# Kernel tuning notes

Hardware: AMD Instinct MI355X
Metric: run time of the kernel (lower is better)

Reference implementation:

```python
import jax, jax.numpy as jnp
import numpy as np

B = 1 << 20
EMB = 8
N_BREEDS, N_TEMPS = 15, 9
HIDDENS = [128, 64, 32]
IN_DIM = (EMB * 2 + 9) * 2  # 50
EPS = 1e-5


def _encode_pet(breed, size, energy, temp, age, social, weight, breed_emb, temp_emb):
    # breed/temp: [B] int -> embedding gather [B,8]; size/energy -> one-hot [B,3]
    be = breed_emb[breed]
    te = temp_emb[temp]
    size_oh = jax.nn.one_hot(size, 3, dtype=be.dtype)
    energy_oh = jax.nn.one_hot(energy, 3, dtype=be.dtype)
    nums = jnp.stack([age / 15.0, social, weight / 100.0], axis=-1)  # [B,3]
    return jnp.concatenate([be, size_oh, energy_oh, te, nums], axis=-1)  # [B,25]


def _mlp(x, Ws, bs, gammas, betas, Wout, bout):
    for W, b, g, bt in zip(Ws, bs, gammas, betas):
        x = x @ W + b
        mu = jnp.mean(x, axis=0)
        var = jnp.mean(jnp.square(x - mu), axis=0)  # biased var (torch BN training)
        x = (x - mu) * jax.lax.rsqrt(var + EPS) * g + bt
        x = jax.nn.relu(x)
    x = x @ Wout + bout
    return jax.nn.sigmoid(x).squeeze(-1)  # [B]


def setup_inputs() -> dict:
    key = jax.random.key(0)
    ks = jax.random.split(key, 32)
    inp = {
        "pet1_breed": jax.random.randint(ks[0], (B,), 0, N_BREEDS, dtype=jnp.int32),
        "pet1_size": jax.random.randint(ks[1], (B,), 0, 3, dtype=jnp.int32),
        "pet1_energy": jax.random.randint(ks[2], (B,), 0, 3, dtype=jnp.int32),
        "pet1_temp": jax.random.randint(ks[3], (B,), 0, N_TEMPS, dtype=jnp.int32),
        "pet1_age": jax.random.uniform(ks[4], (B,)) * 15.0,
        "pet1_social": jax.random.uniform(ks[5], (B,)),
        "pet1_weight": jax.random.uniform(ks[6], (B,)) * 100.0,
        "pet2_breed": jax.random.randint(ks[7], (B,), 0, N_BREEDS, dtype=jnp.int32),
        "pet2_size": jax.random.randint(ks[8], (B,), 0, 3, dtype=jnp.int32),
        "pet2_energy": jax.random.randint(ks[9], (B,), 0, 3, dtype=jnp.int32),
        "pet2_temp": jax.random.randint(ks[10], (B,), 0, N_TEMPS, dtype=jnp.int32),
        "pet2_age": jax.random.uniform(ks[11], (B,)) * 15.0,
        "pet2_social": jax.random.uniform(ks[12], (B,)),
        "pet2_weight": jax.random.uniform(ks[13], (B,)) * 100.0,
        "breed_emb": jax.random.normal(ks[14], (N_BREEDS, EMB), dtype=jnp.float32),
        "temp_emb": jax.random.normal(ks[15], (N_TEMPS, EMB), dtype=jnp.float32),
    }
    prev = IN_DIM
    ki = 16
    for i, h in enumerate(HIDDENS, start=1):
        s = 1.0 / np.sqrt(prev)
        inp[f"W{i}"] = jax.random.uniform(ks[ki], (prev, h), minval=-s, maxval=s); ki += 1
        inp[f"b{i}"] = jax.random.uniform(ks[ki], (h,), minval=-s, maxval=s); ki += 1
        inp[f"gamma{i}"] = jnp.ones((h,), jnp.float32)
        inp[f"beta{i}"] = jnp.zeros((h,), jnp.float32)
        prev = h
    s = 1.0 / np.sqrt(prev)
    inp["W4"] = jax.random.uniform(ks[ki], (prev, 1), minval=-s, maxval=s); ki += 1
    inp["b4"] = jax.random.uniform(ks[ki], (1,), minval=-s, maxval=s)
    return inp


def reference(pet1_breed, pet1_size, pet1_energy, pet1_temp, pet1_age, pet1_social, pet1_weight,
              pet2_breed, pet2_size, pet2_energy, pet2_temp, pet2_age, pet2_social, pet2_weight,
              breed_emb, temp_emb,
              W1, b1, gamma1, beta1, W2, b2, gamma2, beta2, W3, b3, gamma3, beta3, W4, b4):
    f1 = _encode_pet(pet1_breed, pet1_size, pet1_energy, pet1_temp,
                     pet1_age, pet1_social, pet1_weight, breed_emb, temp_emb)
    f2 = _encode_pet(pet2_breed, pet2_size, pet2_energy, pet2_temp,
                     pet2_age, pet2_social, pet2_weight, breed_emb, temp_emb)
    x = jnp.concatenate([f1, f2], axis=-1)  # [B,50]
    return _mlp(x, [W1, W2, W3], [b1, b2, b3], [gamma1, gamma2, gamma3],
                [beta1, beta2, beta3], W4, b4)
```

## Files before the change

kernel.cpp:

```cpp
#include <hip/hip_runtime.h>
#include <hip/hip_bf16.h>

#define BATCH (1u<<20)
static constexpr float EPSBN = 1e-5f;
static constexpr float INV_B = 1.0f / (float)BATCH;

typedef unsigned int   uint;
typedef unsigned short ushort;

#define TSTR 132
#define NTABROWS 66
#define OFF_W2F    55296ULL
#define OFF_W3F    71680ULL
#define OFF_STATS  75776ULL
#define OFF_PARAMS 90112ULL
#define OFF_X2     98304ULL
#define OFF_X3D    (98304ULL + 134217728ULL)
#define T1_NEED    (98304ULL + 134217728ULL)
#define T2_NEED    (98304ULL + 134217728ULL + 67108864ULL)

struct Ptrs {
  const int *br1,*sz1,*en1,*tp1; const float *ag1,*so1,*wt1;
  const int *br2,*sz2,*en2,*tp2; const float *ag2,*so2,*wt2;
  const float *bemb,*temb;
  const float *W1,*b1,*g1,*be1;
  const float *W2,*b2,*g2,*be2;
  const float *W3,*b3,*g3,*be3;
  const float *W4,*b4;
  float* ws; float* out;
};

typedef __attribute__((ext_vector_type(8))) short bf16x8;
typedef __attribute__((ext_vector_type(4))) float f32x4;

__device__ __forceinline__ float4 ld4(const float* p) {
  return *reinterpret_cast<const float4*>(p);
}
__device__ __forceinline__ float4 f4add(float4 a, float4 b) {
  return make_float4(a.x+b.x, a.y+b.y, a.z+b.z, a.w+b.w);
}
__device__ __forceinline__ float4 f4fma(float4 a, float4 w, float s) {
  return make_float4(fmaf(w.x,s,a.x), fmaf(w.y,s,a.y), fmaf(w.z,s,a.z), fmaf(w.w,s,a.w));
}
__device__ __forceinline__ void add4(float4& a, const float4 b) {
  a.x += b.x; a.y += b.y; a.z += b.z; a.w += b.w;
}
__device__ __forceinline__ void fma4s(float4& a, const float4 b, float s) {
  a.x = fmaf(b.x, s, a.x); a.y = fmaf(b.y, s, a.y);
  a.z = fmaf(b.z, s, a.z); a.w = fmaf(b.w, s, a.w);
}

__device__ __forceinline__ ushort bfb(float f) {
  union { __hip_bfloat16 h; ushort u; } cv; cv.h = __float2bfloat16(f); return cv.u;
}
__device__ __forceinline__ uint pk2(float a, float b) {
  return ((uint)bfb(b) << 16) | (uint)bfb(a);
}
__device__ __forceinline__ bf16x8 ldfrag(const void* p) {
  union { uint4 u; bf16x8 v; } cv; cv.u = *reinterpret_cast<const uint4*>(p); return cv.v;
}
__device__ __forceinline__ bf16x8 mkfrag(uint a, uint b, uint c, uint d) {
  union { uint4 u; bf16x8 v; } cv; cv.u = make_uint4(a,b,c,d); return cv.v;
}
__device__ __forceinline__ float bflo(uint w) { return __uint_as_float(w << 16); }
__device__ __forceinline__ float bfhi(uint w) { return __uint_as_float(w & 0xffff0000u); }

struct SIdx { int r[8]; float v[6]; };
__device__ __forceinline__ SIdx load_idx(const Ptrs& P, unsigned s) {
  SIdx o;
  o.r[0] = P.br1[s];      o.r[1] = 15 + P.tp1[s];
  o.r[2] = 24 + P.br2[s]; o.r[3] = 39 + P.tp2[s];
  o.r[4] = 48 + P.sz1[s]; o.r[5] = 51 + P.en1[s];
  o.r[6] = 54 + P.sz2[s]; o.r[7] = 57 + P.en2[s];
  o.v[0] = P.ag1[s]*(1.0f/15.0f); o.v[1] = P.so1[s]; o.v[2] = P.wt1[s]*0.01f;
  o.v[3] = P.ag2[s]*(1.0f/15.0f); o.v[4] = P.so2[s]; o.v[5] = P.wt2[s]*0.01f;
  return o;
}

__device__ __forceinline__ float4 gather4(const float* Tl, const float* contT,
                                          const int rb[8], const float v[6], int c) {
  float4 A = f4add(f4add(ld4(Tl+rb[0]+c), ld4(Tl+rb[1]+c)),
                   f4add(ld4(Tl+rb[2]+c), ld4(Tl+rb[3]+c)));
  float4 B = f4add(f4add(ld4(Tl+rb[4]+c), ld4(Tl+rb[5]+c)),
                   f4add(ld4(Tl+rb[6]+c), ld4(Tl+rb[7]+c)));
  A = f4fma(A, ld4(contT + 60*TSTR + c), v[0]);
  A = f4fma(A, ld4(contT + 61*TSTR + c), v[1]);
  A = f4fma(A, ld4(contT + 62*TSTR + c), v[2]);
  B = f4fma(B, ld4(contT + 63*TSTR + c), v[3]);
  B = f4fma(B, ld4(contT + 64*TSTR + c), v[4]);
  B = f4fma(B, ld4(contT + 65*TSTR + c), v[5]);
  return f4add(A, B);
}

__device__ __forceinline__ void load_rb(const Ptrs& P, unsigned s, int rb[8], float v[6]) {
  SIdx o = load_idx(P, s);
  #pragma unroll
  for (int i = 0; i < 8; ++i) rb[i] = o.r[i]*TSTR;
  #pragma unroll
  for (int i = 0; i < 6; ++i) v[i] = o.v[i];
}

__device__ __forceinline__ void stage_tab(const float* wsT, const float* params,
                                          float* Tl, bool bn1) {
  for (int i = threadIdx.x; i < NTABROWS*TSTR; i += blockDim.x) Tl[i] = wsT[i];
  if (bn1) {
    for (int i = threadIdx.x; i < 128; i += blockDim.x) {
      Tl[66*TSTR + i] = params[i];
      Tl[67*TSTR + i] = params[128 + i];
    }
  }
  __syncthreads();
}

__device__ __forceinline__ void x2_from_lds(const float* Tl, const int rb[8], const float v[6],
                                            const float* W2, const float* b2, float4 acc[16]) {
  #pragma unroll
  for (int j4 = 0; j4 < 16; ++j4) acc[j4] = ld4(b2 + j4*4);
  #pragma unroll 1
  for (int c4 = 0; c4 < 32; ++c4) {
    const int c = c4 * 4;
    float4 x = gather4(Tl, Tl, rb, v, c);
    const float4 sc = *reinterpret_cast<const float4*>(Tl + 66*TSTR + c);
    const float4 sh = *reinterpret_cast<const float4*>(Tl + 67*TSTR + c);
    float hv[4];
    hv[0] = fmaxf(fmaf(x.x, sc.x, sh.x), 0.0f);
    hv[1] = fmaxf(fmaf(x.y, sc.y, sh.y), 0.0f);
    hv[2] = fmaxf(fmaf(x.z, sc.z, sh.z), 0.0f);
    hv[3] = fmaxf(fmaf(x.w, sc.w, sh.w), 0.0f);
    #pragma unroll
    for (int r = 0; r < 4; ++r) {
      const float hr = hv[r];
      const float4* w = reinterpret_cast<const float4*>(W2 + (c + r)*64);
      #pragma unroll
      for (int j4 = 0; j4 < 16; ++j4) fma4s(acc[j4], w[j4], hr);
    }
  }
}

__device__ __forceinline__ void x3_from_acc2(const float4 acc2[16], const Ptrs& P,
                                             const float* sc2, const float* sh2,
                                             float4 acc3[8]) {
  #pragma unroll
  for (int j4 = 0; j4 < 8; ++j4) acc3[j4] = ld4(P.b3 + j4*4);
  #pragma unroll
  for (int k4 = 0; k4 < 16; ++k4) {
    const float4 a = acc2[k4];
    const float4 sc = ld4(sc2 + k4*4), sh = ld4(sh2 + k4*4);
    const float hr[4] = {
      fmaxf(fmaf(a.x, sc.x, sh.x), 0.0f),
      fmaxf(fmaf(a.y, sc.y, sh.y), 0.0f),
      fmaxf(fmaf(a.z, sc.z, sh.z), 0.0f),
      fmaxf(fmaf(a.w, sc.w, sh.w), 0.0f)};
    #pragma unroll
    for (int r = 0; r < 4; ++r) {
      const float4* w = reinterpret_cast<const float4*>(P.W3 + (k4*4 + r)*32);
      #pragma unroll
      for (int j4 = 0; j4 < 8; ++j4) fma4s(acc3[j4], w[j4], hr[r]);
    }
  }
}

__device__ __forceinline__ float bfly_tail32(float st[32], int lane) {
#define BSTEP(D) { const bool h = (lane & D) != 0; \
  _Pragma("unroll") \
  for (int i = 0; i < D; ++i) { \
    float mine = h ? st[i] : st[i+D]; \
    float oth  = __shfl_xor(mine, D, 64); \
    float keep = h ? st[i+D] : st[i]; \
    st[i] = keep + oth; } }
  BSTEP(16) BSTEP(8) BSTEP(4) BSTEP(2) BSTEP(1)
#undef BSTEP
  return st[0];
}

template<bool SQ>
__device__ __forceinline__ float bfly64_from(const float4 acc[16], int lane) {
  float st[32];
  const bool hi = (lane & 32) != 0;
  #pragma unroll
  for (int j4 = 0; j4 < 8; ++j4) {
#define DO1(comp, idx) { \
    float lo = acc[j4].comp, hc = acc[j4+8].comp; \
    if (SQ) { lo *= lo; hc *= hc; } \
    float mine = hi ? lo : hc; \
    float keep = hi ? hc : lo; \
    st[4*j4+idx] = keep + __shfl_xor(mine, 32, 64); }
    DO1(x,0) DO1(y,1) DO1(z,2) DO1(w,3)
#undef DO1
  }
  return bfly_tail32(st, lane);
}

template<bool SQ>
__device__ __forceinline__ float bfly32_from(const float4 acc3[8], int lane) {
  float st[32];
  const bool hi = (lane & 32) != 0;
  #pragma unroll
  for (int j4 = 0; j4 < 8; ++j4) {
#define DO1(comp, idx) { \
    float vv = acc3[j4].comp; \
    if (SQ) vv *= vv; \
    float mine = hi ? vv : 0.0f; \
    float keep = hi ? 0.0f : vv; \
    st[4*j4+idx] = keep + __shfl_xor(mine, 32, 64); }
    DO1(x,0) DO1(y,1) DO1(z,2) DO1(w,3)
#undef DO1
  }
  return bfly_tail32(st, lane);
}


__global__ __launch_bounds__(256) void k_prep(Ptrs P) {
  const int t = threadIdx.x;
  float* T = P.ws;
  {
    float* st = (float*)((char*)P.ws + OFF_STATS);
    for (int i = t; i < 224*16; i += 256) st[i] = 0.0f;
  }
  if (t < 128) {
    const int c = t;
    for (int b = 0; b < 15; ++b) {
      float a1 = P.b1[c], a2 = 0.0f;
      #pragma unroll
      for (int e = 0; e < 8; ++e) {
        a1 = fmaf(P.bemb[b*8+e], P.W1[e*128 + c], a1);
        a2 = fmaf(P.bemb[b*8+e], P.W1[(25+e)*128 + c], a2);
      }
      T[b*TSTR + c] = a1; T[(24+b)*TSTR + c] = a2;
    }
    for (int tt = 0; tt < 9; ++tt) {
      float a1 = 0.0f, a2 = 0.0f;
      #pragma unroll
      for (int e = 0; e < 8; ++e) {
        a1 = fmaf(P.temb[tt*8+e], P.W1[(14+e)*128 + c], a1);
        a2 = fmaf(P.temb[tt*8+e], P.W1[(39+e)*128 + c], a2);
      }
      T[(15+tt)*TSTR + c] = a1; T[(39+tt)*TSTR + c] = a2;
    }
    #pragma unroll
    for (int i = 0; i < 3; ++i) {
      T[(48+i)*TSTR + c] = P.W1[(8+i)*128 + c];
      T[(51+i)*TSTR + c] = P.W1[(11+i)*128 + c];
      T[(54+i)*TSTR + c] = P.W1[(33+i)*128 + c];
      T[(57+i)*TSTR + c] = P.W1[(36+i)*128 + c];
    }
    const int cr[6] = {22,23,24,47,48,49};
    #pragma unroll
    for (int m = 0; m < 6; ++m) T[(60+m)*TSTR + c] = P.W1[cr[m]*128 + c];
  }
  __syncthreads();
  __hip_bfloat16* w2f = (__hip_bfloat16*)((char*)P.ws + OFF_W2F);
  for (int slot = t; slot < 1024; slot += 256) {
    const int fid = slot >> 6, l = slot & 63;
    const int mt = fid >> 2, kk = fid & 3, q = l >> 4, m = l & 15;
    #pragma unroll
    for (int e = 0; e < 8; ++e)
      w2f[slot*8 + e] = __float2bfloat16(P.W2[(kk*32 + 8*q + e)*64 + 16*mt + m]);
  }
  __hip_bfloat16* w3f = (__hip_bfloat16*)((char*)P.ws + OFF_W3F);
  for (int slot = t; slot < 256; slot += 256) {
    const int fid = slot >> 6, l = slot & 63;
    const int mt = fid >> 1, kk = fid & 1, q = l >> 4, m = l & 15;
    #pragma unroll
    for (int e = 0; e < 8; ++e)
      w3f[slot*8 + e] = __float2bfloat16(P.W3[(kk*32 + 8*q + e)*32 + 16*mt + m]);
  }
}

__global__ __launch_bounds__(512) void k_stats1(Ptrs P) {
  __shared__ __align__(16) float Tl[60*TSTR];
  __shared__ float sred[256];
  for (int i = threadIdx.x; i < 60*TSTR; i += 512) Tl[i] = P.ws[i];
  if (threadIdx.x < 256) sred[threadIdx.x] = 0.f;
  __syncthreads();
  const int lane = threadIdx.x & 63;
  const int q = lane >> 4, m16 = lane & 15;
  const float* contT = P.ws;
  const unsigned gw = (blockIdx.x*512 + threadIdx.x) >> 6;
  const unsigned nw = (gridDim.x*512) >> 6;
  const int kk = gw & 3;
  const int c = kk*32 + 8*q;
  const unsigned NT = BATCH >> 4;
  unsigned it = gw >> 2;
  const unsigned ts = nw >> 2;
  float4 sa = make_float4(0,0,0,0), sb = sa, qa = sa, qb = sa;
  bool active = it < NT;
  SIdx cur;
  if (active) cur = load_idx(P, it*16 + m16);
  while (active) {
    const unsigned itn = it + ts;
    const bool more = itn < NT;
    SIdx nxt;
    if (more) nxt = load_idx(P, itn*16 + m16);
    int rb[8];
    #pragma unroll
    for (int i = 0; i < 8; ++i) rb[i] = cur.r[i]*TSTR;
    const float4 xa = gather4(Tl, contT, rb, cur.v, c);
    const float4 xb = gather4(Tl, contT, rb, cur.v, c + 4);
    add4(sa, xa); add4(sb, xb);
    qa.x = fmaf(xa.x, xa.x, qa.x); qa.y = fmaf(xa.y, xa.y, qa.y);
    qa.z = fmaf(xa.z, xa.z, qa.z); qa.w = fmaf(xa.w, xa.w, qa.w);
    qb.x = fmaf(xb.x, xb.x, qb.x); qb.y = fmaf(xb.y, xb.y, qb.y);
    qb.z = fmaf(xb.z, xb.z, qb.z); qb.w = fmaf(xb.w, xb.w, qb.w);
    if (!more) break;
    cur = nxt; it = itn;
  }
  #pragma unroll
  for (int d = 1; d <= 8; d <<= 1) {
    sa.x += __shfl_xor(sa.x, d, 64); sa.y += __shfl_xor(sa.y, d, 64);
    sa.z += __shfl_xor(sa.z, d, 64); sa.w += __shfl_xor(sa.w, d, 64);
    sb.x += __shfl_xor(sb.x, d, 64); sb.y += __shfl_xor(sb.y, d, 64);
    sb.z += __shfl_xor(sb.z, d, 64); sb.w += __shfl_xor(sb.w, d, 64);
    qa.x += __shfl_xor(qa.x, d, 64); qa.y += __shfl_xor(qa.y, d, 64);
    qa.z += __shfl_xor(qa.z, d, 64); qa.w += __shfl_xor(qa.w, d, 64);
    qb.x += __shfl_xor(qb.x, d, 64); qb.y += __shfl_xor(qb.y, d, 64);
    qb.z += __shfl_xor(qb.z, d, 64); qb.w += __shfl_xor(qb.w, d, 64);
  }
  if (m16 == 0) {
    atomicAdd(&sred[c+0], sa.x); atomicAdd(&sred[c+1], sa.y);
    atomicAdd(&sred[c+2], sa.z); atomicAdd(&sred[c+3], sa.w);
    atomicAdd(&sred[c+4], sb.x); atomicAdd(&sred[c+5], sb.y);
    atomicAdd(&sred[c+6], sb.z); atomicAdd(&sred[c+7], sb.w);
    atomicAdd(&sred[128+c+0], qa.x); atomicAdd(&sred[128+c+1], qa.y);
    atomicAdd(&sred[128+c+2], qa.z); atomicAdd(&sred[128+c+3], qa.w);
    atomicAdd(&sred[128+c+4], qb.x); atomicAdd(&sred[128+c+5], qb.y);
    atomicAdd(&sred[128+c+6], qb.z); atomicAdd(&sred[128+c+7], qb.w);
  }
  __syncthreads();
  if (threadIdx.x < 128) {
    float* stat = (float*)((char*)P.ws + OFF_STATS) + (size_t)threadIdx.x*16;
    atomicAdd(stat,     sred[threadIdx.x]);
    atomicAdd(stat + 8, sred[128+threadIdx.x]);
  }
}

__global__ void k_finalize(Ptrs P, int nch, int entry0, int pofs,
                           const float* g, const float* be) {
  const int c = threadIdx.x;
  if (c >= nch) return;
  const float* stat = (const float*)((const char*)P.ws + OFF_STATS) + (size_t)(entry0 + c)*16;
  const float mean = stat[0] * INV_B;
  const float var  = stat[8] * INV_B - mean*mean;
  const float inv  = 1.0f / sqrtf(var + EPSBN);
  const float scale = g[c] * inv;
  float* params = (float*)((char*)P.ws + OFF_PARAMS);
  params[pofs + c]       = scale;
  params[pofs + nch + c] = be[c] - mean * scale;
}

__global__ __launch_bounds__(512) void k_l2m(Ptrs P) {
  __shared__ __align__(16) float Tl[60*TSTR];
  __shared__ __align__(16) float bn[256];
  __shared__ float sred[128];
  for (int i = threadIdx.x; i < 60*TSTR; i += 512) Tl[i] = P.ws[i];
  if (threadIdx.x < 128) {
    const float* stat = (const float*)((const char*)P.ws + OFF_STATS) + (size_t)threadIdx.x*16;
    const float mean = stat[0] * INV_B;
    const float var  = stat[8] * INV_B - mean*mean;
    const float scale = P.g1[threadIdx.x] / sqrtf(var + EPSBN);
    bn[threadIdx.x]       = scale;
    bn[128 + threadIdx.x] = P.be1[threadIdx.x] - mean * scale;
    sred[threadIdx.x] = 0.f;
  }
  __syncthreads();
  const float* contT = P.ws;
  const int lane = threadIdx.x & 63;
  const int q = lane >> 4, m16 = lane & 15;
  const char* w2fB = (const char*)P.ws + OFF_W2F;
  char* x2B = (char*)P.ws + OFF_X2;
  const unsigned nw = (gridDim.x*512) >> 6;
  const unsigned NT = BATCH >> 4;
  unsigned it = (blockIdx.x*512 + threadIdx.x) >> 6;
  f32x4 ssum[4], ssq[4];
  #pragma unroll
  for (int mt = 0; mt < 4; ++mt) { ssum[mt] = (f32x4){0,0,0,0}; ssq[mt] = (f32x4){0,0,0,0}; }
  bool active = it < NT;
  SIdx cur;
  if (active) cur = load_idx(P, it*16 + m16);
  while (active) {
    const unsigned itn = it + nw;
    const bool more = itn < NT;
    SIdx nxt;
    if (more) nxt = load_idx(P, itn*16 + m16);
    const unsigned s = it*16 + m16;
    int rb[8];
    #pragma unroll
    for (int i = 0; i < 8; ++i) rb[i] = cur.r[i]*TSTR;
    f32x4 D[4];
    #pragma unroll
    for (int mt = 0; mt < 4; ++mt) {
      const float4 b = ld4(P.b2 + 16*mt + 4*q);
      D[mt][0] = b.x; D[mt][1] = b.y; D[mt][2] = b.z; D[mt][3] = b.w;
    }
    #pragma unroll
    for (int kk = 0; kk < 4; ++kk) {
      const int c = kk*32 + 8*q;
      const float4 xa = gather4(Tl, contT, rb, cur.v, c);
      const float4 xb = gather4(Tl, contT, rb, cur.v, c + 4);
      const float4 sca = ld4(bn + c), sha = ld4(bn + 128 + c);
      const float4 scb = ld4(bn + c + 4), shb = ld4(bn + 128 + c + 4);
      const float h0 = fmaxf(fmaf(xa.x, sca.x, sha.x), 0.f);
      const float h1 = fmaxf(fmaf(xa.y, sca.y, sha.y), 0.f);
      const float h2 = fmaxf(fmaf(xa.z, sca.z, sha.z), 0.f);
      const float h3 = fmaxf(fmaf(xa.w, sca.w, sha.w), 0.f);
      const float h4 = fmaxf(fmaf(xb.x, scb.x, shb.x), 0.f);
      const float h5 = fmaxf(fmaf(xb.y, scb.y, shb.y), 0.f);
      const float h6 = fmaxf(fmaf(xb.z, scb.z, shb.z), 0.f);
      const float h7 = fmaxf(fmaf(xb.w, scb.w, shb.w), 0.f);
      const bf16x8 bf = mkfrag(pk2(h0,h1), pk2(h2,h3), pk2(h4,h5), pk2(h6,h7));
      #pragma unroll
      for (int mt = 0; mt < 4; ++mt) {
        const bf16x8 af = ldfrag(w2fB + (size_t)((mt*4+kk)*64 + lane)*16);
        D[mt] = __builtin_amdgcn_mfma_f32_16x16x32_bf16(af, bf, D[mt], 0, 0, 0);
      }
    }
    #pragma unroll
    for (int mt = 0; mt < 4; ++mt) {
      #pragma unroll
      for (int r = 0; r < 4; ++r) {
        const float d = D[mt][r];
        ssum[mt][r] += d;
        ssq[mt][r]   = fmaf(d, d, ssq[mt][r]);
      }
      const uint lo = pk2(D[mt][0], D[mt][1]);
      const uint hi = pk2(D[mt][2], D[mt][3]);
      *reinterpret_cast<uint2*>(x2B + (size_t)s*128 + (16*mt + 4*q)*2) = make_uint2(lo, hi);
    }
    if (!more) break;
    cur = nxt; it = itn;
  }
  #pragma unroll
  for (int d = 1; d <= 8; d <<= 1) {
    #pragma unroll
    for (int mt = 0; mt < 4; ++mt) {
      #pragma unroll
      for (int r = 0; r < 4; ++r) {
        ssum[mt][r] += __shfl_xor(ssum[mt][r], d, 64);
        ssq[mt][r]  += __shfl_xor(ssq[mt][r],  d, 64);
      }
    }
  }
  if (m16 == 0) {
    #pragma unroll
    for (int mt = 0; mt < 4; ++mt) {
      #pragma unroll
      for (int r = 0; r < 4; ++r) {
        const int ch = 16*mt + 4*q + r;
        atomicAdd(&sred[ch], ssum[mt][r]);
        atomicAdd(&sred[64+ch], ssq[mt][r]);
      }
    }
  }
  __syncthreads();
  if (threadIdx.x < 64) {
    float* stat = (float*)((char*)P.ws + OFF_STATS) + (size_t)(128 + threadIdx.x)*16;
    atomicAdd(stat, sred[threadIdx.x]);
    atomicAdd(stat + 8, sred[64+threadIdx.x]);
  }
}

__global__ __launch_bounds__(256) void k_l3m(Ptrs P, int dense) {
  __shared__ __align__(16) float bn[128];
  __shared__ float sred[64];
  if (threadIdx.x < 64) {
    const float* stat = (const float*)((const char*)P.ws + OFF_STATS) + (size_t)(128 + threadIdx.x)*16;
    const float mean = stat[0] * INV_B;
    const float var  = stat[8] * INV_B - mean*mean;
    const float scale = P.g2[threadIdx.x] / sqrtf(var + EPSBN);
    bn[threadIdx.x]      = scale;
    bn[64 + threadIdx.x] = P.be2[threadIdx.x] - mean * scale;
    sred[threadIdx.x] = 0.f;
  }
  __syncthreads();
  const int lane = threadIdx.x & 63;
  const int q = lane >> 4, m16 = lane & 15;
  const char* w3fB = (const char*)P.ws + OFF_W3F;
  const char* xB = (const char*)P.ws + OFF_X2;
  char* x3B = dense ? ((char*)P.ws + OFF_X3D) : ((char*)P.ws + OFF_X2);
  const size_t x3str = dense ? 64 : 128;
  const unsigned nw = (gridDim.x*256) >> 6;
  const unsigned NT = BATCH >> 4;
  unsigned it = (blockIdx.x*256 + threadIdx.x) >> 6;
  f32x4 ssum[2], ssq[2];
  #pragma unroll
  for (int mt = 0; mt < 2; ++mt) { ssum[mt] = (f32x4){0,0,0,0}; ssq[mt] = (f32x4){0,0,0,0}; }
  bool active = it < NT;
  unsigned s = it*16 + m16;
  uint4 u0, u1;
  if (active) {
    u0 = *reinterpret_cast<const uint4*>(xB + (size_t)s*128 + q*16);
    u1 = *reinterpret_cast<const uint4*>(xB + (size_t)s*128 + 64 + q*16);
  }
  while (active) {
    const unsigned itn = it + nw;
    const bool more = itn < NT;
    uint4 n0, n1;
    if (more) {
      const unsigned sn = itn*16 + m16;
      n0 = *reinterpret_cast<const uint4*>(xB + (size_t)sn*128 + q*16);
      n1 = *reinterpret_cast<const uint4*>(xB + (size_t)sn*128 + 64 + q*16);
    }
    f32x4 D[2];
    #pragma unroll
    for (int mt = 0; mt < 2; ++mt) {
      const float4 b = ld4(P.b3 + 16*mt + 4*q);
      D[mt][0] = b.x; D[mt][1] = b.y; D[mt][2] = b.z; D[mt][3] = b.w;
    }
    #pragma unroll
    for (int kk = 0; kk < 2; ++kk) {
      const uint4 u = (kk == 0) ? u0 : u1;
      const int c = kk*32 + 8*q;
      const float4 scA = ld4(bn + c), shA = ld4(bn + 64 + c);
      const float4 scB = ld4(bn + c + 4), shB = ld4(bn + 64 + c + 4);
      const uint w[4] = {u.x,u.y,u.z,u.w};
      const float h0 = fmaxf(fmaf(bflo(w[0]), scA.x, shA.x), 0.f);
      const float h1 = fmaxf(fmaf(bfhi(w[0]), scA.y, shA.y), 0.f);
      const float h2 = fmaxf(fmaf(bflo(w[1]), scA.z, shA.z), 0.f);
      const float h3 = fmaxf(fmaf(bfhi(w[1]), scA.w, shA.w), 0.f);
      const float h4 = fmaxf(fmaf(bflo(w[2]), scB.x, shB.x), 0.f);
      const float h5 = fmaxf(fmaf(bfhi(w[2]), scB.y, shB.y), 0.f);
      const float h6 = fmaxf(fmaf(bflo(w[3]), scB.z, shB.z), 0.f);
      const float h7 = fmaxf(fmaf(bfhi(w[3]), scB.w, shB.w), 0.f);
      const bf16x8 bf = mkfrag(pk2(h0,h1), pk2(h2,h3), pk2(h4,h5), pk2(h6,h7));
      #pragma unroll
      for (int mt = 0; mt < 2; ++mt) {
        const bf16x8 af = ldfrag(w3fB + (size_t)((mt*2+kk)*64 + lane)*16);
        D[mt] = __builtin_amdgcn_mfma_f32_16x16x32_bf16(af, bf, D[mt], 0, 0, 0);
      }
    }
    #pragma unroll
    for (int mt = 0; mt < 2; ++mt) {
      #pragma unroll
      for (int r = 0; r < 4; ++r) {
        const float d = D[mt][r];
        ssum[mt][r] += d;
        ssq[mt][r]   = fmaf(d, d, ssq[mt][r]);
      }
      const uint lo = pk2(D[mt][0], D[mt][1]);
      const uint hi = pk2(D[mt][2], D[mt][3]);
      *reinterpret_cast<uint2*>(x3B + (size_t)s*x3str + (16*mt + 4*q)*2) = make_uint2(lo, hi);
    }
    if (!more) break;
    u0 = n0; u1 = n1; it = itn; s = it*16 + m16;
  }
  #pragma unroll
  for (int d = 1; d <= 8; d <<= 1) {
    #pragma unroll
    for (int mt = 0; mt < 2; ++mt) {
      #pragma unroll
      for (int r = 0; r < 4; ++r) {
        ssum[mt][r] += __shfl_xor(ssum[mt][r], d, 64);
        ssq[mt][r]  += __shfl_xor(ssq[mt][r],  d, 64);
      }
    }
  }
  if (m16 == 0) {
    #pragma unroll
    for (int mt = 0; mt < 2; ++mt) {
      #pragma unroll
      for (int r = 0; r < 4; ++r) {
        const int ch = 16*mt + 4*q + r;
        atomicAdd(&sred[ch], ssum[mt][r]);
        atomicAdd(&sred[32+ch], ssq[mt][r]);
      }
    }
  }
  __syncthreads();
  if (threadIdx.x < 32) {
    float* stat = (float*)((char*)P.ws + OFF_STATS) + (size_t)(192 + threadIdx.x)*16;
    atomicAdd(stat, sred[threadIdx.x]);
    atomicAdd(stat + 8, sred[32+threadIdx.x]);
  }
}

__global__ __launch_bounds__(256) void k_l4n(Ptrs P, int dense) {
  __shared__ float bn[64];
  if (threadIdx.x < 32) {
    const float* stat = (const float*)((const char*)P.ws + OFF_STATS) + (size_t)(192 + threadIdx.x)*16;
    const float mean = stat[0] * INV_B;
    const float var  = stat[8] * INV_B - mean*mean;
    const float scale = P.g3[threadIdx.x] / sqrtf(var + EPSBN);
    bn[threadIdx.x]      = scale;
    bn[32 + threadIdx.x] = P.be3[threadIdx.x] - mean * scale;
  }
  __syncthreads();
  const float* sc3 = bn, *sh3 = bn + 32;
  const char* xB = dense ? ((const char*)P.ws + OFF_X3D) : ((const char*)P.ws + OFF_X2);
  const size_t xstr = dense ? 64 : 128;
  const unsigned stride = gridDim.x * 256;
  for (unsigned s = blockIdx.x*256 + threadIdx.x; s < BATCH; s += stride) {
    float z = P.b4[0];
    #pragma unroll
    for (int c16 = 0; c16 < 4; ++c16) {
      const uint4 u = *reinterpret_cast<const uint4*>(xB + (size_t)s*xstr + c16*16);
      const uint w[4] = {u.x,u.y,u.z,u.w};
      #pragma unroll
      for (int j = 0; j < 4; ++j) {
        const int ch = c16*8 + 2*j;
        const float hlo = fmaxf(fmaf(bflo(w[j]), sc3[ch],   sh3[ch]),   0.f);
        const float hhi = fmaxf(fmaf(bfhi(w[j]), sc3[ch+1], sh3[ch+1]), 0.f);
        z = fmaf(hlo, P.W4[ch], z);
        z = fmaf(hhi, P.W4[ch+1], z);
      }
    }
    P.out[s] = 1.0f / (1.0f + __expf(-z));
  }
}

__global__ __launch_bounds__(256) void k_l2r(Ptrs P) {
  __shared__ __align__(16) float Tl[68*TSTR];
  __shared__ float red[512];
  const float* params = (const float*)((const char*)P.ws + OFF_PARAMS);
  stage_tab(P.ws, params, Tl, true);
  const int lane = threadIdx.x & 63;
  float4 sums[16], sqs[16];
  #pragma unroll
  for (int j4 = 0; j4 < 16; ++j4) {
    sums[j4] = make_float4(0.f,0.f,0.f,0.f);
    sqs[j4]  = make_float4(0.f,0.f,0.f,0.f);
  }
  const unsigned stride = gridDim.x * 256;
  for (unsigned s = blockIdx.x*256 + threadIdx.x; s < BATCH; s += stride) {
    int rb[8]; float v[6];
    load_rb(P, s, rb, v);
    float4 acc[16];
    x2_from_lds(Tl, rb, v, P.W2, P.b2, acc);
    #pragma unroll
    for (int j4 = 0; j4 < 16; ++j4) {
      add4(sums[j4], acc[j4]);
      sqs[j4].x = fmaf(acc[j4].x, acc[j4].x, sqs[j4].x);
      sqs[j4].y = fmaf(acc[j4].y, acc[j4].y, sqs[j4].y);
      sqs[j4].z = fmaf(acc[j4].z, acc[j4].z, sqs[j4].z);
      sqs[j4].w = fmaf(acc[j4].w, acc[j4].w, sqs[j4].w);
    }
  }
  const float psum = bfly64_from<false>(sums, lane);
  const float psq  = bfly64_from<false>(sqs,  lane);
  red[threadIdx.x] = psum; red[256 + threadIdx.x] = psq;
  __syncthreads();
  const int t = threadIdx.x;
  if (t < 64) {
    const float s0 = red[t] + red[t+64] + red[t+128] + red[t+192];
    const float q0 = red[256+t] + red[256+t+64] + red[256+t+128] + red[256+t+192];
    float* stat = (float*)((char*)P.ws + OFF_STATS) + (size_t)(128 + t)*16;
    atomicAdd(stat, s0); atomicAdd(stat + 8, q0);
  }
}

__global__ __launch_bounds__(256) void k_l3_rec(Ptrs P) {
  __shared__ __align__(16) float Tl[68*TSTR];
  __shared__ float red[512];
  const float* params = (const float*)((const char*)P.ws + OFF_PARAMS);
  stage_tab(P.ws, params, Tl, true);
  const float* sc2 = params + 256, *sh2 = params + 320;
  const int lane = threadIdx.x & 63;
  float4 sums3[8], sqs3[8];
  #pragma unroll
  for (int j4 = 0; j4 < 8; ++j4) {
    sums3[j4] = make_float4(0.f,0.f,0.f,0.f);
    sqs3[j4]  = make_float4(0.f,0.f,0.f,0.f);
  }
  const unsigned stride = gridDim.x * 256;
  for (unsigned s = blockIdx.x*256 + threadIdx.x; s < BATCH; s += stride) {
    int rb[8]; float v[6];
    load_rb(P, s, rb, v);
    float4 acc2[16];
    x2_from_lds(Tl, rb, v, P.W2, P.b2, acc2);
    float4 acc3[8];
    x3_from_acc2(acc2, P, sc2, sh2, acc3);
    #pragma unroll
    for (int j4 = 0; j4 < 8; ++j4) {
      add4(sums3[j4], acc3[j4]);
      sqs3[j4].x = fmaf(acc3[j4].x, acc3[j4].x, sqs3[j4].x);
      sqs3[j4].y = fmaf(acc3[j4].y, acc3[j4].y, sqs3[j4].y);
      sqs3[j4].z = fmaf(acc3[j4].z, acc3[j4].z, sqs3[j4].z);
      sqs3[j4].w = fmaf(acc3[j4].w, acc3[j4].w, sqs3[j4].w);
    }
  }
  const float psum = bfly32_from<false>(sums3, lane);
  const float psq  = bfly32_from<false>(sqs3,  lane);
  red[threadIdx.x] = psum; red[256 + threadIdx.x] = psq;
  __syncthreads();
  const int t = threadIdx.x;
  if (t < 32) {
    const float s0 = red[t] + red[t+64] + red[t+128] + red[t+192];
    const float q0 = red[256+t] + red[256+t+64] + red[256+t+128] + red[256+t+192];
    float* stat = (float*)((char*)P.ws + OFF_STATS) + (size_t)(192 + t)*16;
    atomicAdd(stat, s0); atomicAdd(stat + 8, q0);
  }
}

__global__ __launch_bounds__(256) void k_l4_rec(Ptrs P) {
  __shared__ __align__(16) float Tl[68*TSTR];
  const float* params = (const float*)((const char*)P.ws + OFF_PARAMS);
  stage_tab(P.ws, params, Tl, true);
  const float* sc2 = params + 256, *sh2 = params + 320;
  const float* sc3 = params + 384, *sh3 = params + 416;
  const unsigned stride = gridDim.x * 256;
  for (unsigned s = blockIdx.x*256 + threadIdx.x; s < BATCH; s += stride) {
    int rb[8]; float v[6];
    load_rb(P, s, rb, v);
    float4 acc2[16];
    x2_from_lds(Tl, rb, v, P.W2, P.b2, acc2);
    float4 acc3[8];
    x3_from_acc2(acc2, P, sc2, sh2, acc3);
    float z = P.b4[0];
    #pragma unroll
    for (int k4 = 0; k4 < 8; ++k4) {
      const float4 a = acc3[k4];
      const float4 sc = ld4(sc3 + k4*4), sh = ld4(sh3 + k4*4);
      z = fmaf(fmaxf(fmaf(a.x, sc.x, sh.x), 0.0f), P.W4[k4*4+0], z);
      z = fmaf(fmaxf(fmaf(a.y, sc.y, sh.y), 0.0f), P.W4[k4*4+1], z);
      z = fmaf(fmaxf(fmaf(a.z, sc.z, sh.z), 0.0f), P.W4[k4*4+2], z);
      z = fmaf(fmaxf(fmaf(a.w, sc.w, sh.w), 0.0f), P.W4[k4*4+3], z);
    }
    P.out[s] = 1.0f / (1.0f + __expf(-z));
  }
}


extern "C" void kernel_launch(void* const* d_in, const int* in_sizes, int n_in,
                              void* d_out, int out_size, void* d_ws, size_t ws_size,
                              hipStream_t stream) {
  Ptrs P;
  P.br1 = (const int*)d_in[0];  P.sz1 = (const int*)d_in[1];
  P.en1 = (const int*)d_in[2];  P.tp1 = (const int*)d_in[3];
  P.ag1 = (const float*)d_in[4]; P.so1 = (const float*)d_in[5]; P.wt1 = (const float*)d_in[6];
  P.br2 = (const int*)d_in[7];  P.sz2 = (const int*)d_in[8];
  P.en2 = (const int*)d_in[9];  P.tp2 = (const int*)d_in[10];
  P.ag2 = (const float*)d_in[11]; P.so2 = (const float*)d_in[12]; P.wt2 = (const float*)d_in[13];
  P.bemb = (const float*)d_in[14]; P.temb = (const float*)d_in[15];
  P.W1 = (const float*)d_in[16]; P.b1 = (const float*)d_in[17];
  P.g1 = (const float*)d_in[18]; P.be1 = (const float*)d_in[19];
  P.W2 = (const float*)d_in[20]; P.b2 = (const float*)d_in[21];
  P.g2 = (const float*)d_in[22]; P.be2 = (const float*)d_in[23];
  P.W3 = (const float*)d_in[24]; P.b3 = (const float*)d_in[25];
  P.g3 = (const float*)d_in[26]; P.be3 = (const float*)d_in[27];
  P.W4 = (const float*)d_in[28]; P.b4 = (const float*)d_in[29];
  P.ws = (float*)d_ws; P.out = (float*)d_out;

  const bool t1 = ws_size >= T1_NEED;
  const int dense = (ws_size >= T2_NEED) ? 1 : 0;

  hipLaunchKernelGGL(k_prep, dim3(1), dim3(256), 0, stream, P);
  hipLaunchKernelGGL(k_stats1, dim3(1024), dim3(512), 0, stream, P);
  if (t1) {
    hipLaunchKernelGGL(k_l2m, dim3(1024), dim3(512), 0, stream, P);
    hipLaunchKernelGGL(k_l3m, dim3(2048), dim3(256), 0, stream, P, dense);
    hipLaunchKernelGGL(k_l4n, dim3(2048), dim3(256), 0, stream, P, dense);
  } else {
    hipLaunchKernelGGL(k_finalize, dim3(1), dim3(128), 0, stream, P, 128, 0, 0, P.g1, P.be1);
    hipLaunchKernelGGL(k_l2r, dim3(1024), dim3(256), 0, stream, P);
    hipLaunchKernelGGL(k_finalize, dim3(1), dim3(64), 0, stream, P, 64, 128, 256, P.g2, P.be2);
    hipLaunchKernelGGL(k_l3_rec, dim3(1024), dim3(256), 0, stream, P);
    hipLaunchKernelGGL(k_finalize, dim3(1), dim3(32), 0, stream, P, 32, 192, 384, P.g3, P.be3);
    hipLaunchKernelGGL(k_l4_rec, dim3(2048), dim3(256), 0, stream, P);
  }
}
```

Before: 693.6 us.

## Split BN statistics out of layer 2/3 GEMM kernels into separate stat-reduction kernels

Removes the per-thread sum and sum-of-squares accumulation, shuffle reduction and shared/global atomics from the layer-2 and layer-3 MFMA kernels. Two new kernels re-read the stored bf16 activations and compute the batch-norm statistics. This frees registers and instructions in the GEMM kernels and moves the statistics onto the rounded bf16 values, at the cost of an extra full read of the activation buffers and two more launches.

After: 606.6 us. 12.5% less time.

```diff
diff --git a/kernel.cpp b/kernel.cpp
--- a/kernel.cpp
+++ b/kernel.cpp
@@ -351,7 +351,6 @@
 __global__ __launch_bounds__(512) void k_l2m(Ptrs P) {
   __shared__ __align__(16) float Tl[60*TSTR];
   __shared__ __align__(16) float bn[256];
-  __shared__ float sred[128];
   for (int i = threadIdx.x; i < 60*TSTR; i += 512) Tl[i] = P.ws[i];
   if (threadIdx.x < 128) {
     const float* stat = (const float*)((const char*)P.ws + OFF_STATS) + (size_t)threadIdx.x*16;
@@ -360,7 +359,6 @@
     const float scale = P.g1[threadIdx.x] / sqrtf(var + EPSBN);
     bn[threadIdx.x]       = scale;
     bn[128 + threadIdx.x] = P.be1[threadIdx.x] - mean * scale;
-    sred[threadIdx.x] = 0.f;
   }
   __syncthreads();
   const float* contT = P.ws;
@@ -371,13 +369,9 @@
   const unsigned nw = (gridDim.x*512) >> 6;
   const unsigned NT = BATCH >> 4;
   unsigned it = (blockIdx.x*512 + threadIdx.x) >> 6;
-  f32x4 ssum[4], ssq[4];
-  #pragma unroll
-  for (int mt = 0; mt < 4; ++mt) { ssum[mt] = (f32x4){0,0,0,0}; ssq[mt] = (f32x4){0,0,0,0}; }
-  bool active = it < NT;
-  SIdx cur;
-  if (active) cur = load_idx(P, it*16 + m16);
-  while (active) {
+  if (it >= NT) return;
+  SIdx cur = load_idx(P, it*16 + m16);
+  while (true) {
     const unsigned itn = it + nw;
     const bool more = itn < NT;
     SIdx nxt;
@@ -416,12 +410,6 @@
     }
     #pragma unroll
     for (int mt = 0; mt < 4; ++mt) {
-      #pragma unroll
-      for (int r = 0; r < 4; ++r) {
-        const float d = D[mt][r];
-        ssum[mt][r] += d;
-        ssq[mt][r]   = fmaf(d, d, ssq[mt][r]);
-      }
       const uint lo = pk2(D[mt][0], D[mt][1]);
       const uint hi = pk2(D[mt][2], D[mt][3]);
       *reinterpret_cast<uint2*>(x2B + (size_t)s*128 + (16*mt + 4*q)*2) = make_uint2(lo, hi);
@@ -429,39 +417,42 @@
     if (!more) break;
     cur = nxt; it = itn;
   }
-  #pragma unroll
-  for (int d = 1; d <= 8; d <<= 1) {
-    #pragma unroll
-    for (int mt = 0; mt < 4; ++mt) {
-      #pragma unroll
-      for (int r = 0; r < 4; ++r) {
-        ssum[mt][r] += __shfl_xor(ssum[mt][r], d, 64);
-        ssq[mt][r]  += __shfl_xor(ssq[mt][r],  d, 64);
-      }
-    }
-  }
-  if (m16 == 0) {
-    #pragma unroll
-    for (int mt = 0; mt < 4; ++mt) {
-      #pragma unroll
-      for (int r = 0; r < 4; ++r) {
-        const int ch = 16*mt + 4*q + r;
-        atomicAdd(&sred[ch], ssum[mt][r]);
-        atomicAdd(&sred[64+ch], ssq[mt][r]);
-      }
-    }
+}
+
+__global__ __launch_bounds__(256) void k_stats2(Ptrs P) {
+  const uint* x2u = (const uint*)((const char*)P.ws + OFF_X2);
+  const int pid = threadIdx.x & 31;
+  const int lane = threadIdx.x & 63;
+  const int w = threadIdx.x >> 6;
+  float slo = 0.f, shi = 0.f, qlo = 0.f, qhi = 0.f;
+  const unsigned r0 = blockIdx.x*8 + (threadIdx.x >> 5);
+  const unsigned rs = gridDim.x*8;
+  #pragma unroll 4
+  for (unsigned r = r0; r < BATCH; r += rs) {
+    const uint u = x2u[(size_t)r*32 + pid];
+    const float lo = bflo(u), hi = bfhi(u);
+    slo += lo; shi += hi;
+    qlo = fmaf(lo, lo, qlo); qhi = fmaf(hi, hi, qhi);
+  }
+  slo += __shfl_xor(slo, 32, 64); shi += __shfl_xor(shi, 32, 64);
+  qlo += __shfl_xor(qlo, 32, 64); qhi += __shfl_xor(qhi, 32, 64);
+  __shared__ float red[512];
+  if (lane < 32) {
+    red[w*64 + 2*pid]       = slo; red[w*64 + 2*pid + 1]       = shi;
+    red[256 + w*64 + 2*pid] = qlo; red[256 + w*64 + 2*pid + 1] = qhi;
   }
   __syncthreads();
   if (threadIdx.x < 64) {
-    float* stat = (float*)((char*)P.ws + OFF_STATS) + (size_t)(128 + threadIdx.x)*16;
-    atomicAdd(stat, sred[threadIdx.x]);
-    atomicAdd(stat + 8, sred[64+threadIdx.x]);
+    const int c = threadIdx.x;
+    const float s  = red[c] + red[64+c] + red[128+c] + red[192+c];
+    const float qq = red[256+c] + red[320+c] + red[384+c] + red[448+c];
+    float* stat = (float*)((char*)P.ws + OFF_STATS) + (size_t)(128 + c)*16;
+    atomicAdd(stat, s); atomicAdd(stat + 8, qq);
   }
 }
 
 __global__ __launch_bounds__(256) void k_l3m(Ptrs P, int dense) {
   __shared__ __align__(16) float bn[128];
-  __shared__ float sred[64];
   if (threadIdx.x < 64) {
     const float* stat = (const float*)((const char*)P.ws + OFF_STATS) + (size_t)(128 + threadIdx.x)*16;
     const float mean = stat[0] * INV_B;
@@ -469,7 +460,6 @@
     const float scale = P.g2[threadIdx.x] / sqrtf(var + EPSBN);
     bn[threadIdx.x]      = scale;
     bn[64 + threadIdx.x] = P.be2[threadIdx.x] - mean * scale;
-    sred[threadIdx.x] = 0.f;
   }
   __syncthreads();
   const int lane = threadIdx.x & 63;
@@ -481,17 +471,11 @@
   const unsigned nw = (gridDim.x*256) >> 6;
   const unsigned NT = BATCH >> 4;
   unsigned it = (blockIdx.x*256 + threadIdx.x) >> 6;
-  f32x4 ssum[2], ssq[2];
-  #pragma unroll
-  for (int mt = 0; mt < 2; ++mt) { ssum[mt] = (f32x4){0,0,0,0}; ssq[mt] = (f32x4){0,0,0,0}; }
-  bool active = it < NT;
+  if (it >= NT) return;
   unsigned s = it*16 + m16;
-  uint4 u0, u1;
-  if (active) {
-    u0 = *reinterpret_cast<const uint4*>(xB + (size_t)s*128 + q*16);
-    u1 = *reinterpret_cast<const uint4*>(xB + (size_t)s*128 + 64 + q*16);
-  }
-  while (active) {
+  uint4 u0 = *reinterpret_cast<const uint4*>(xB + (size_t)s*128 + q*16);
+  uint4 u1 = *reinterpret_cast<const uint4*>(xB + (size_t)s*128 + 64 + q*16);
+  while (true) {
     const unsigned itn = it + nw;
     const bool more = itn < NT;
     uint4 n0, n1;
@@ -530,12 +514,6 @@
     }
     #pragma unroll
     for (int mt = 0; mt < 2; ++mt) {
-      #pragma unroll
-      for (int r = 0; r < 4; ++r) {
-        const float d = D[mt][r];
-        ssum[mt][r] += d;
-        ssq[mt][r]   = fmaf(d, d, ssq[mt][r]);
-      }
       const uint lo = pk2(D[mt][0], D[mt][1]);
       const uint hi = pk2(D[mt][2], D[mt][3]);
       *reinterpret_cast<uint2*>(x3B + (size_t)s*x3str + (16*mt + 4*q)*2) = make_uint2(lo, hi);
@@ -543,33 +521,42 @@
     if (!more) break;
     u0 = n0; u1 = n1; it = itn; s = it*16 + m16;
   }
-  #pragma unroll
-  for (int d = 1; d <= 8; d <<= 1) {
-    #pragma unroll
-    for (int mt = 0; mt < 2; ++mt) {
-      #pragma unroll
-      for (int r = 0; r < 4; ++r) {
-        ssum[mt][r] += __shfl_xor(ssum[mt][r], d, 64);
-        ssq[mt][r]  += __shfl_xor(ssq[mt][r],  d, 64);
-      }
-    }
-  }
-  if (m16 == 0) {
-    #pragma unroll
-    for (int mt = 0; mt < 2; ++mt) {
-      #pragma unroll
-      for (int r = 0; r < 4; ++r) {
-        const int ch = 16*mt + 4*q + r;
-        atomicAdd(&sred[ch], ssum[mt][r]);
-        atomicAdd(&sred[32+ch], ssq[mt][r]);
-      }
-    }
+}
+
+__global__ __launch_bounds__(256) void k_stats3(Ptrs P, int dense) {
+  const uint* xu = dense ? (const uint*)((const char*)P.ws + OFF_X3D)
+                         : (const uint*)((const char*)P.ws + OFF_X2);
+  const unsigned rstr = dense ? 16 : 32;
+  const int pid = threadIdx.x & 15;
+  const int lane = threadIdx.x & 63;
+  const int w = threadIdx.x >> 6;
+  float slo = 0.f, shi = 0.f, qlo = 0.f, qhi = 0.f;
+  const unsigned r0 = blockIdx.x*16 + (threadIdx.x >> 4);
+  const unsigned rs = gridDim.x*16;
+  #pragma unroll 4
+  for (unsigned r = r0; r < BATCH; r += rs) {
+    const uint u = xu[(size_t)r*rstr + pid];
+    const float lo = bflo(u), hi = bfhi(u);
+    slo += lo; shi += hi;
+    qlo = fmaf(lo, lo, qlo); qhi = fmaf(hi, hi, qhi);
+  }
+  #pragma unroll
+  for (int d = 16; d <= 32; d <<= 1) {
+    slo += __shfl_xor(slo, d, 64); shi += __shfl_xor(shi, d, 64);
+    qlo += __shfl_xor(qlo, d, 64); qhi += __shfl_xor(qhi, d, 64);
+  }
+  __shared__ float red[256];
+  if (lane < 16) {
+    red[w*32 + 2*pid]       = slo; red[w*32 + 2*pid + 1]       = shi;
+    red[128 + w*32 + 2*pid] = qlo; red[128 + w*32 + 2*pid + 1] = qhi;
   }
   __syncthreads();
   if (threadIdx.x < 32) {
-    float* stat = (float*)((char*)P.ws + OFF_STATS) + (size_t)(192 + threadIdx.x)*16;
-    atomicAdd(stat, sred[threadIdx.x]);
-    atomicAdd(stat + 8, sred[32+threadIdx.x]);
+    const int c = threadIdx.x;
+    const float s  = red[c] + red[32+c] + red[64+c] + red[96+c];
+    const float qq = red[128+c] + red[160+c] + red[192+c] + red[224+c];
+    float* stat = (float*)((char*)P.ws + OFF_STATS) + (size_t)(192 + c)*16;
+    atomicAdd(stat, s); atomicAdd(stat + 8, qq);
   }
 }
 
@@ -746,7 +733,9 @@
   hipLaunchKernelGGL(k_stats1, dim3(1024), dim3(512), 0, stream, P);
   if (t1) {
     hipLaunchKernelGGL(k_l2m, dim3(1024), dim3(512), 0, stream, P);
+    hipLaunchKernelGGL(k_stats2, dim3(1024), dim3(256), 0, stream, P);
     hipLaunchKernelGGL(k_l3m, dim3(2048), dim3(256), 0, stream, P, dense);
+    hipLaunchKernelGGL(k_stats3, dim3(1024), dim3(256), 0, stream, P, dense);
     hipLaunchKernelGGL(k_l4n, dim3(2048), dim3(256), 0, stream, P, dense);
   } else {
     hipLaunchKernelGGL(k_finalize, dim3(1), dim3(128), 0, stream, P, 128, 0, 0, P.g1, P.be1);
```
